# Optimization experiments

Measured on AMD Instinct MI355X. Metric: run time of the kernel, lower is better.

## Reference

```python
import jax, jax.numpy as jnp
import numpy as np

LORA_RANK = 16
LORA_ALPHA = 32.0
LORA_SCALE = LORA_ALPHA / LORA_RANK
W_BITS = 8
A_BITS = 8


def fake_quant(x, bits):
    """Symmetric per-tensor fake quantization with straight-through estimator."""
    qmax = 2.0 ** (bits - 1) - 1.0
    scale = jnp.maximum(jnp.max(jnp.abs(x)), 1e-8) / qmax
    q = jnp.clip(jnp.round(x / scale), -qmax, qmax) * scale
    return x + jax.lax.stop_gradient(q - x)  # STE


def quant_linear_lora(x, W, b, A, B):
    # x: [..., in], W: [out, in], A: [r, in], B: [out, r]
    xq = fake_quant(x, A_BITS)
    Wq = fake_quant(W, W_BITS)
    base = jnp.einsum('bsi,oi->bso', xq, Wq) + b
    lora = jnp.einsum('bsr,or->bso', jnp.einsum('bsi,ri->bsr', x, A), B)
    return base + LORA_SCALE * lora


def setup_inputs() -> dict:
    key = jax.random.key(0)
    ks = jax.random.split(key, 9)
    n_embd, d_ff, B_, S = 1024, 4096, 4, 2048
    s_in = 1.0 / np.sqrt(n_embd)
    s_ff = 1.0 / np.sqrt(d_ff)
    return {
        'hidden_states': jax.random.normal(ks[0], (B_, S, n_embd), jnp.float32),
        'W_fc': jax.random.normal(ks[1], (d_ff, n_embd), jnp.float32) * s_in,
        'b_fc': jax.random.normal(ks[2], (d_ff,), jnp.float32) * 0.02,
        'A_fc': jax.random.normal(ks[3], (LORA_RANK, n_embd), jnp.float32) * s_in,
        'B_fc': jax.random.normal(ks[4], (d_ff, LORA_RANK), jnp.float32) * 0.01,
        'W_proj': jax.random.normal(ks[5], (n_embd, d_ff), jnp.float32) * s_ff,
        'b_proj': jax.random.normal(ks[6], (n_embd,), jnp.float32) * 0.02,
        'A_proj': jax.random.normal(ks[7], (LORA_RANK, d_ff), jnp.float32) * s_ff,
        'B_proj': jax.random.normal(ks[8], (n_embd, LORA_RANK), jnp.float32) * 0.01,
    }


def reference(hidden_states, W_fc, b_fc, A_fc, B_fc, W_proj, b_proj, A_proj, B_proj):
    h = quant_linear_lora(hidden_states, W_fc, b_fc, A_fc, B_fc)
    h = jax.nn.gelu(h, approximate=False)  # nn.GELU() default = exact erf GELU
    h = quant_linear_lora(h, W_proj, b_proj, A_proj, B_proj)
    return h
```

## Files before the change

### kernel.cpp

```cpp
#include <hip/hip_runtime.h>
#include <stdint.h>

using i32x4 = __attribute__((ext_vector_type(4))) int;
using f32x4 = __attribute__((ext_vector_type(4))) float;
using f16x4 = __attribute__((ext_vector_type(4))) _Float16;

#define M_TOK 8192
#define N_EMB 1024
#define D_FF  4096

__device__ __forceinline__ void async_lds16(void* lds, const void* g) {
  __builtin_amdgcn_global_load_lds(
      (const __attribute__((address_space(1))) void*)g,
      (__attribute__((address_space(3))) void*)lds, 16, 0, 0);
}

__global__ void zero_slots_k(unsigned* s) {
  if (threadIdx.x < 16) s[threadIdx.x] = 0u;
}

__global__ void absmax_k(const float* __restrict__ p, long n, unsigned* __restrict__ slot) {
  long i = ((long)blockIdx.x * blockDim.x + threadIdx.x) * 4;
  long stride = (long)gridDim.x * blockDim.x * 4;
  float m = 0.f;
  for (; i < n; i += stride) {
    float4 v = *(const float4*)(p + i);
    m = fmaxf(m, fmaxf(fmaxf(fabsf(v.x), fabsf(v.y)), fmaxf(fabsf(v.z), fabsf(v.w))));
  }
  for (int o = 32; o; o >>= 1) m = fmaxf(m, __shfl_xor(m, o));
  __shared__ float sm[4];
  if ((threadIdx.x & 63) == 0) sm[threadIdx.x >> 6] = m;
  __syncthreads();
  if (threadIdx.x == 0) {
    m = fmaxf(fmaxf(sm[0], sm[1]), fmaxf(sm[2], sm[3]));
    atomicMax(slot, __float_as_uint(m));
  }
}

__global__ void quant_k(const float* __restrict__ p, int8_t* __restrict__ q, long n,
                        const unsigned* __restrict__ slot) {
  float inv = 127.f / fmaxf(__uint_as_float(*slot), 1e-8f);
  long i = ((long)blockIdx.x * blockDim.x + threadIdx.x) * 4;
  long stride = (long)gridDim.x * blockDim.x * 4;
  for (; i < n; i += stride) {
    float4 v = *(const float4*)(p + i);
    int b0 = (int)fminf(fmaxf(rintf(v.x * inv), -127.f), 127.f);
    int b1 = (int)fminf(fmaxf(rintf(v.y * inv), -127.f), 127.f);
    int b2 = (int)fminf(fmaxf(rintf(v.z * inv), -127.f), 127.f);
    int b3 = (int)fminf(fmaxf(rintf(v.w * inv), -127.f), 127.f);
    int w = (b0 & 0xff) | ((b1 & 0xff) << 8) | ((b2 & 0xff) << 16) | ((b3 & 0xff) << 24);
    *(int*)(q + i) = w;
  }
}

__global__ void prep_bfrag_k(const float* __restrict__ A, _Float16* __restrict__ Bp, int K) {
  int s = blockIdx.x;
  int l = threadIdx.x;
  int r = l & 15, g = l >> 4;
  float4 v = *(const float4*)(A + (long)r * K + s * 16 + g * 4);
  f16x4 h;
  h[0] = (_Float16)v.x; h[1] = (_Float16)v.y; h[2] = (_Float16)v.z; h[3] = (_Float16)v.w;
  *(f16x4*)(Bp + ((long)s * 64 + l) * 4) = h;
}

__global__ __launch_bounds__(512) void lora_quant_k(
    const float* __restrict__ X, const _Float16* __restrict__ Bpre,
    const unsigned* __restrict__ slot, int8_t* __restrict__ Q,
    float* __restrict__ T, int K) {
  int lane = threadIdx.x & 63, wave = threadIdx.x >> 6;
  int row0 = blockIdx.x * 16;
  int r = lane & 15, g = lane >> 4;
  float inv = 127.f / fmaxf(__uint_as_float(*slot), 1e-8f);

  int kPerWave = K >> 3;
  int kbase = wave * kPerWave;
  const float* xrow = X + (long)(row0 + r) * K;
  int8_t* qrow = Q + (long)(row0 + r) * K;

  f32x4 acc = {0.f, 0.f, 0.f, 0.f};
  int nsteps = kPerWave >> 4;
#pragma unroll 4
  for (int s = 0; s < nsteps; s++) {
    int k = kbase + s * 16 + g * 4;
    float4 v = *(const float4*)(xrow + k);
    int b0 = (int)fminf(fmaxf(rintf(v.x * inv), -127.f), 127.f);
    int b1 = (int)fminf(fmaxf(rintf(v.y * inv), -127.f), 127.f);
    int b2 = (int)fminf(fmaxf(rintf(v.z * inv), -127.f), 127.f);
    int b3 = (int)fminf(fmaxf(rintf(v.w * inv), -127.f), 127.f);
    *(int*)(qrow + k) = (b0 & 0xff) | ((b1 & 0xff) << 8) | ((b2 & 0xff) << 16) | ((b3 & 0xff) << 24);
    f16x4 a;
    a[0] = (_Float16)v.x; a[1] = (_Float16)v.y; a[2] = (_Float16)v.z; a[3] = (_Float16)v.w;
    int gs = (kbase + s * 16) >> 4;
    f16x4 b = *(const f16x4*)(Bpre + ((long)gs * 64 + lane) * 4);
    acc = __builtin_amdgcn_mfma_f32_16x16x16f16(a, b, acc, 0, 0, 0);
  }

  __shared__ float part[8][16][17];
#pragma unroll
  for (int j = 0; j < 4; j++) part[wave][g * 4 + j][r] = acc[j];
  __syncthreads();
  int t = threadIdx.x;
  if (t < 256) {
    int m = t >> 4, rr = t & 15;
    float sum = 0.f;
#pragma unroll
    for (int w = 0; w < 8; w++) sum += part[w][m][rr];
    T[(long)(row0 + m) * 16 + rr] = 2.0f * sum;
  }
}

template <bool GELU>
__global__ __launch_bounds__(256, 2) void gemm_q8(
    const int8_t* __restrict__ Aq, const int8_t* __restrict__ Bq,
    int M, int N, int K,
    const unsigned* __restrict__ sa, const unsigned* __restrict__ sb,
    const float* __restrict__ bias,
    const float* __restrict__ T,
    const float* __restrict__ Bl,
    float* __restrict__ C, unsigned* hmax) {
  __shared__ __align__(16) int8_t lds[65536];

  int nwg = gridDim.x * gridDim.y;
  int lid = blockIdx.y * gridDim.x + blockIdx.x;
  int q8 = nwg >> 3;
  int nid = (lid & 7) * q8 + (lid >> 3);
  int bn = (nid % gridDim.x) * 128;
  int bm = (nid / gridDim.x) * 128;

  int t = threadIdx.x;
  int lane = t & 63, wave = t >> 6;
  int wr = wave >> 1, wc = wave & 1;
  int l16 = lane & 15, lq = lane >> 4;

  int ldst[4];
  const int8_t* srcA[4];
  const int8_t* srcB[4];
#pragma unroll
  for (int i = 0; i < 4; i++) {
    int s = i * 256 + t;
    int row = s >> 3;
    int cg = (t & 7) ^ (row & 7);
    ldst[i] = s * 16;
    srcA[i] = Aq + (long)(bm + row) * K + cg * 16;
    srcB[i] = Bq + (long)(bn + row) * K + cg * 16;
  }

  int aoff[4][2], boff[4][2];
#pragma unroll
  for (int mf = 0; mf < 4; mf++) {
    int row = wr * 64 + mf * 16 + l16;
#pragma unroll
    for (int kh = 0; kh < 2; kh++) {
      int c = kh * 4 + lq;
      aoff[mf][kh] = row * 128 + ((c ^ (row & 7)) << 4);
    }
  }
#pragma unroll
  for (int nf = 0; nf < 4; nf++) {
    int row = wc * 64 + nf * 16 + l16;
#pragma unroll
    for (int kh = 0; kh < 2; kh++) {
      int c = kh * 4 + lq;
      boff[nf][kh] = row * 128 + ((c ^ (row & 7)) << 4);
    }
  }

  i32x4 acc[4][4] = {};
  int KT = K >> 7;

  {
#pragma unroll
    for (int i = 0; i < 4; i++) {
      async_lds16(lds + ldst[i], srcA[i]);
      async_lds16(lds + 16384 + ldst[i], srcB[i]);
    }
  }
  __syncthreads();

  int cur = 0;
  for (int kt = 0; kt < KT; kt++) {
    if (kt + 1 < KT) {
      long ko = (long)(kt + 1) * 128;
      const int8_t* A_l_next_dummy;
      (void)A_l_next_dummy;
      int nb = (cur ^ 1) * 32768;
#pragma unroll
      for (int i = 0; i < 4; i++) {
        async_lds16(lds + nb + ldst[i], srcA[i] + ko);
        async_lds16(lds + nb + 16384 + ldst[i], srcB[i] + ko);
      }
    }

    const int8_t* A_l = lds + cur * 32768;
    const int8_t* B_l = A_l + 16384;
#pragma unroll
    for (int kh = 0; kh < 2; kh++) {
      i32x4 av[4], bv[4];
#pragma unroll
      for (int mf = 0; mf < 4; mf++) av[mf] = *(const i32x4*)(A_l + aoff[mf][kh]);
#pragma unroll
      for (int nf = 0; nf < 4; nf++) bv[nf] = *(const i32x4*)(B_l + boff[nf][kh]);
      __builtin_amdgcn_s_setprio(1);
#pragma unroll
      for (int mf = 0; mf < 4; mf++)
#pragma unroll
        for (int nf = 0; nf < 4; nf++)
          acc[mf][nf] = __builtin_amdgcn_mfma_i32_16x16x64_i8(av[mf], bv[nf], acc[mf][nf], 0, 0, 0);
      __builtin_amdgcn_s_setprio(0);
    }
    __syncthreads();
    cur ^= 1;
  }

  float s = (fmaxf(__uint_as_float(*sa), 1e-8f) * (1.f / 127.f)) *
            (fmaxf(__uint_as_float(*sb), 1e-8f) * (1.f / 127.f));

  f16x4 af[4], bf[4];
#pragma unroll
  for (int mf = 0; mf < 4; mf++) {
    int m = bm + wr * 64 + mf * 16 + l16;
    float4 tv = *(const float4*)(T + (long)m * 16 + lq * 4);
    f16x4 v; v[0] = (_Float16)tv.x; v[1] = (_Float16)tv.y; v[2] = (_Float16)tv.z; v[3] = (_Float16)tv.w;
    af[mf] = v;
  }
#pragma unroll
  for (int nf = 0; nf < 4; nf++) {
    int n = bn + wc * 64 + nf * 16 + l16;
    float4 bv4 = *(const float4*)(Bl + (long)n * 16 + lq * 4);
    f16x4 v; v[0] = (_Float16)bv4.x; v[1] = (_Float16)bv4.y; v[2] = (_Float16)bv4.z; v[3] = (_Float16)bv4.w;
    bf[nf] = v;
  }
  float bias_v[4];
#pragma unroll
  for (int nf = 0; nf < 4; nf++) bias_v[nf] = bias[bn + wc * 64 + nf * 16 + l16];

  float lmax = 0.f;
#pragma unroll
  for (int mf = 0; mf < 4; mf++) {
#pragma unroll
    for (int nf = 0; nf < 4; nf++) {
      f32x4 fa = __builtin_amdgcn_mfma_f32_16x16x16f16(af[mf], bf[nf], f32x4{0.f, 0.f, 0.f, 0.f}, 0, 0, 0);
      int n = bn + wc * 64 + nf * 16 + l16;
#pragma unroll
      for (int j = 0; j < 4; j++) {
        int m = bm + wr * 64 + mf * 16 + lq * 4 + j;
        float v = s * (float)acc[mf][nf][j] + bias_v[nf] + fa[j];
        if constexpr (GELU) {
          v = 0.5f * v * (1.0f + erff(v * 0.70710678118654752f));
          lmax = fmaxf(lmax, fabsf(v));
        }
        C[(long)m * N + n] = v;
      }
    }
  }
  if constexpr (GELU) {
    for (int o = 32; o; o >>= 1) lmax = fmaxf(lmax, __shfl_xor(lmax, o));
    if (lane == 0) atomicMax(hmax, __float_as_uint(lmax));
  }
}

extern "C" void kernel_launch(void* const* d_in, const int* in_sizes, int n_in,
                              void* d_out, int out_size, void* d_ws, size_t ws_size,
                              hipStream_t stream) {
  const float* x   = (const float*)d_in[0];
  const float* Wfc = (const float*)d_in[1];
  const float* bfc = (const float*)d_in[2];
  const float* Afc = (const float*)d_in[3];
  const float* Bfc = (const float*)d_in[4];
  const float* Wpj = (const float*)d_in[5];
  const float* bpj = (const float*)d_in[6];
  const float* Apj = (const float*)d_in[7];
  const float* Bpj = (const float*)d_in[8];
  float* out = (float*)d_out;

  char* ws = (char*)d_ws;
  unsigned* slots = (unsigned*)ws;
  int8_t* qx  = (int8_t*)(ws + 256);
  int8_t* qwf = qx  + (size_t)M_TOK * N_EMB;
  int8_t* qwp = qwf + (size_t)D_FF * N_EMB;
  int8_t* qh  = qwp + (size_t)N_EMB * D_FF;
  float*  t1  = (float*)(qh + (size_t)M_TOK * D_FF);
  float*  t2  = t1  + (size_t)M_TOK * 16;
  _Float16* Bp1 = (_Float16*)(t2 + (size_t)M_TOK * 16);
  _Float16* Bp2 = Bp1 + (size_t)N_EMB * 16;
  float*  h   = (float*)(Bp2 + (size_t)D_FF * 16);

  zero_slots_k<<<1, 64, 0, stream>>>(slots);
  absmax_k<<<1024, 256, 0, stream>>>(x,   (long)M_TOK * N_EMB, slots + 0);
  absmax_k<<<1024, 256, 0, stream>>>(Wfc, (long)D_FF * N_EMB,  slots + 1);
  absmax_k<<<1024, 256, 0, stream>>>(Wpj, (long)N_EMB * D_FF,  slots + 2);

  quant_k<<<2048, 256, 0, stream>>>(Wfc, qwf, (long)D_FF * N_EMB, slots + 1);
  quant_k<<<2048, 256, 0, stream>>>(Wpj, qwp, (long)N_EMB * D_FF, slots + 2);

  prep_bfrag_k<<<N_EMB / 16, 64, 0, stream>>>(Afc, Bp1, N_EMB);
  prep_bfrag_k<<<D_FF / 16, 64, 0, stream>>>(Apj, Bp2, D_FF);

  lora_quant_k<<<M_TOK / 16, 512, 0, stream>>>(x, Bp1, slots + 0, qx, t1, N_EMB);

  gemm_q8<true><<<dim3(D_FF / 128, M_TOK / 128), 256, 0, stream>>>(
      qx, qwf, M_TOK, D_FF, N_EMB, slots + 0, slots + 1, bfc, t1, Bfc, h, slots + 3);

  lora_quant_k<<<M_TOK / 16, 512, 0, stream>>>(h, Bp2, slots + 3, qh, t2, D_FF);

  gemm_q8<false><<<dim3(N_EMB / 128, M_TOK / 128), 256, 0, stream>>>(
      qh, qwp, M_TOK, N_EMB, D_FF, slots + 3, slots + 2, bpj, t2, Bpj, out, nullptr);
}
```

Before: 305.9 us.

## Replace double-buffered int8 GEMM with single-buffer loop at higher occupancy

Removes the LDS double buffer and prefetch of the next K tile, halving shared memory to 32KB so that three workgroups can be resident per CU (launch bounds raised to 3). It also drops the XCD-aware block-index remapping and the s_setprio hints, and restructures the swizzled LDS offsets to a single array XORed per K half. The trade-off is that global-to-LDS loads are no longer overlapped with MFMA work within a workgroup and must rely on other resident workgroups to hide latency. Removing the block remapping may also hurt L2 locality across XCDs.

```diff
diff --git a/kernel.cpp b/kernel.cpp
--- a/kernel.cpp
+++ b/kernel.cpp
@@ -110,7 +110,7 @@
 }
 
 template <bool GELU>
-__global__ __launch_bounds__(256, 2) void gemm_q8(
+__global__ __launch_bounds__(256, 3) void gemm_q8(
     const int8_t* __restrict__ Aq, const int8_t* __restrict__ Bq,
     int M, int N, int K,
     const unsigned* __restrict__ sa, const unsigned* __restrict__ sb,
@@ -118,14 +118,11 @@
     const float* __restrict__ T,
     const float* __restrict__ Bl,
     float* __restrict__ C, unsigned* hmax) {
-  __shared__ __align__(16) int8_t lds[65536];
-
-  int nwg = gridDim.x * gridDim.y;
-  int lid = blockIdx.y * gridDim.x + blockIdx.x;
-  int q8 = nwg >> 3;
-  int nid = (lid & 7) * q8 + (lid >> 3);
-  int bn = (nid % gridDim.x) * 128;
-  int bm = (nid / gridDim.x) * 128;
+  __shared__ __align__(16) int8_t As[16384];
+  __shared__ __align__(16) int8_t Bs[16384];
+
+  int bn = blockIdx.x * 128;
+  int bm = blockIdx.y * 128;
 
   int t = threadIdx.x;
   int lane = t & 63, wave = t >> 6;
@@ -139,77 +136,50 @@
   for (int i = 0; i < 4; i++) {
     int s = i * 256 + t;
     int row = s >> 3;
-    int cg = (t & 7) ^ (row & 7);
+    int cg = (s & 7) ^ (row & 7);
     ldst[i] = s * 16;
     srcA[i] = Aq + (long)(bm + row) * K + cg * 16;
     srcB[i] = Bq + (long)(bn + row) * K + cg * 16;
   }
 
-  int aoff[4][2], boff[4][2];
+  int aoff[4], boff[4];
 #pragma unroll
   for (int mf = 0; mf < 4; mf++) {
     int row = wr * 64 + mf * 16 + l16;
-#pragma unroll
-    for (int kh = 0; kh < 2; kh++) {
-      int c = kh * 4 + lq;
-      aoff[mf][kh] = row * 128 + ((c ^ (row & 7)) << 4);
-    }
+    aoff[mf] = row * 128 + ((lq ^ (row & 7)) << 4);
   }
 #pragma unroll
   for (int nf = 0; nf < 4; nf++) {
     int row = wc * 64 + nf * 16 + l16;
-#pragma unroll
-    for (int kh = 0; kh < 2; kh++) {
-      int c = kh * 4 + lq;
-      boff[nf][kh] = row * 128 + ((c ^ (row & 7)) << 4);
-    }
+    boff[nf] = row * 128 + ((lq ^ (row & 7)) << 4);
   }
 
   i32x4 acc[4][4] = {};
   int KT = K >> 7;
 
-  {
-#pragma unroll
-    for (int i = 0; i < 4; i++) {
-      async_lds16(lds + ldst[i], srcA[i]);
-      async_lds16(lds + 16384 + ldst[i], srcB[i]);
-    }
-  }
-  __syncthreads();
-
-  int cur = 0;
-  for (int kt = 0; kt < KT; kt++) {
-    if (kt + 1 < KT) {
-      long ko = (long)(kt + 1) * 128;
-      const int8_t* A_l_next_dummy;
-      (void)A_l_next_dummy;
-      int nb = (cur ^ 1) * 32768;
-#pragma unroll
-      for (int i = 0; i < 4; i++) {
-        async_lds16(lds + nb + ldst[i], srcA[i] + ko);
-        async_lds16(lds + nb + 16384 + ldst[i], srcB[i] + ko);
-      }
-    }
-
-    const int8_t* A_l = lds + cur * 32768;
-    const int8_t* B_l = A_l + 16384;
+  for (int kt = 0; kt < KT; ++kt) {
+    long ko = (long)kt * 128;
+#pragma unroll
+    for (int i = 0; i < 4; i++) async_lds16(As + ldst[i], srcA[i] + ko);
+#pragma unroll
+    for (int i = 0; i < 4; i++) async_lds16(Bs + ldst[i], srcB[i] + ko);
+    __syncthreads();
+
 #pragma unroll
     for (int kh = 0; kh < 2; kh++) {
+      int kx = kh << 6;
       i32x4 av[4], bv[4];
 #pragma unroll
-      for (int mf = 0; mf < 4; mf++) av[mf] = *(const i32x4*)(A_l + aoff[mf][kh]);
-#pragma unroll
-      for (int nf = 0; nf < 4; nf++) bv[nf] = *(const i32x4*)(B_l + boff[nf][kh]);
-      __builtin_amdgcn_s_setprio(1);
+      for (int mf = 0; mf < 4; mf++) av[mf] = *(const i32x4*)(As + (aoff[mf] ^ kx));
+#pragma unroll
+      for (int nf = 0; nf < 4; nf++) bv[nf] = *(const i32x4*)(Bs + (boff[nf] ^ kx));
 #pragma unroll
       for (int mf = 0; mf < 4; mf++)
 #pragma unroll
         for (int nf = 0; nf < 4; nf++)
           acc[mf][nf] = __builtin_amdgcn_mfma_i32_16x16x64_i8(av[mf], bv[nf], acc[mf][nf], 0, 0, 0);
-      __builtin_amdgcn_s_setprio(0);
     }
     __syncthreads();
-    cur ^= 1;
   }
 
   float s = (fmaxf(__uint_as_float(*sa), 1e-8f) * (1.f / 127.f)) *
```

New measurement: 303.0 us. About the same (-0.9%).
